# Optimization experiments

Measured on AMD Instinct MI355X. Metric: run time of the kernel, lower is better.

## Reference

```python
import jax, jax.numpy as jnp
import numpy as np

NO_LAYERS = 2048
MODES = 4096
APL = 8          # action_per_layer
BATCH = 1        # forced to 1 by the final .view on a batch-1 tensor


def setup_inputs() -> dict:
    key = jax.random.key(0)
    ks = jax.random.split(key, 12)

    def cplx(k, shape):
        k1, k2 = jax.random.split(k)
        return (jax.random.uniform(k1, shape) + 1j * jax.random.uniform(k2, shape)).astype(jnp.complex64)

    return {
        "model_p": jax.random.normal(ks[0], (NO_LAYERS, MODES), dtype=jnp.float32),
        # complex spectral weights, torch.rand init on cfloat -> uniform real+imag
        "w_fft_0": cplx(ks[1], (1, MODES)),
        "w_fft_1": cplx(ks[2], (1, MODES)),
        "w_fft_2": cplx(ks[3], (1, MODES)),
        # lin1: no_layers -> modes
        "lin1_w": jax.random.normal(ks[4], (MODES, NO_LAYERS), dtype=jnp.float32) / np.sqrt(NO_LAYERS),
        "lin1_b": jnp.zeros((MODES,), dtype=jnp.float32),
        # lin2: modes -> no_layers * action_per_layer  (the big matvec, 268 MB)
        "lin2_w": jax.random.normal(ks[5], (NO_LAYERS * APL, MODES), dtype=jnp.float32) / np.sqrt(MODES),
        "lin2_b": jnp.zeros((NO_LAYERS * APL,), dtype=jnp.float32),
    }


def _space_time_fft_feature(data, w_fft):
    # data: (b, f, p) real or complex; w_fft: (1, modes) complex
    fft_data = jnp.fft.fft(data, norm='forward')                 # (b, f, p)
    # einsum contracts both p and n, leaving singleton m -> (b, f, 1)
    y = jnp.einsum('bfp,mn->bfm', fft_data, w_fft)
    iffw = jnp.fft.ifft(y, norm='forward')                       # (b, f, 1)
    return jnp.tanh(iffw).real                                   # complex tanh, take real


def reference(model_p, w_fft_0, w_fft_1, w_fft_2, lin1_w, lin1_b, lin2_w, lin2_b):
    x = _space_time_fft_feature(model_p[None], w_fft_0)          # (1, no_layers, 1)
    x = _space_time_fft_feature(x, w_fft_1)                      # (1, no_layers, 1)
    x = _space_time_fft_feature(x, w_fft_2)                      # (1, no_layers, 1)
    x = x.reshape(1, -1)                                         # (1, no_layers)
    x = jnp.tanh(x @ lin1_w.T + lin1_b)                          # (1, modes)
    x = (x @ lin2_w.T + lin2_b).reshape(BATCH, NO_LAYERS, APL)   # (1, no_layers, apl)
    return x
```

## Files before the change

kernel.cpp:

```cpp
#include <hip/hip_runtime.h>
#include <math.h>

#define NO_LAYERS 2048
#define MODES 4096
#define APL 8
#define OUT_N (NO_LAYERS * APL)

typedef float nf4 __attribute__((ext_vector_type(4)));

__device__ __forceinline__ float retanh_cplx(float t, float Sr, float Si) {
    float x = t * Sr;
    float y = t * Si;
    float a = 2.0f * fabsf(x);
    float e1 = expf(-a);
    float e2 = e1 * e1;
    float num = 1.0f - e2;
    float den = 1.0f + e2 + 2.0f * e1 * cosf(2.0f * y);
    return copysignf(num / den, x);
}

__global__ void __launch_bounds__(256) k_lin1f(const float* __restrict__ model_p,
                                               const float* __restrict__ w0,
                                               const float* __restrict__ w1,
                                               const float* __restrict__ w2,
                                               const float* __restrict__ w,
                                               const float* __restrict__ b,
                                               float* __restrict__ h) {
    __shared__ float red[3][2][4];
    __shared__ float S[3][2];
    __shared__ float ts[NO_LAYERS];
    const int tid = threadIdx.x;
    const int wave = tid >> 6, lane = tid & 63;

    const int row = blockIdx.x * 4 + wave;
    const nf4* wp = (const nf4*)(w + (size_t)row * NO_LAYERS);
    nf4 wv[(NO_LAYERS / 4) / 64];
    #pragma unroll
    for (int i = 0; i < (NO_LAYERS / 4) / 64; i++)
        wv[i] = __builtin_nontemporal_load(&wp[i * 64 + lane]);

    const float* wptr[3] = {w0, w1, w2};
    float sr[3] = {0.f, 0.f, 0.f}, si[3] = {0.f, 0.f, 0.f};
    #pragma unroll
    for (int q = 0; q < 3; q++) {
        const float2* p = (const float2*)wptr[q];
        #pragma unroll
        for (int i = 0; i < MODES / 256; i++) {
            float2 v = p[i * 256 + tid];
            sr[q] += v.x; si[q] += v.y;
        }
    }
    #pragma unroll
    for (int off = 32; off > 0; off >>= 1) {
        #pragma unroll
        for (int q = 0; q < 3; q++) {
            sr[q] += __shfl_down(sr[q], off);
            si[q] += __shfl_down(si[q], off);
        }
    }
    if (lane == 0) {
        #pragma unroll
        for (int q = 0; q < 3; q++) { red[q][0][wave] = sr[q]; red[q][1][wave] = si[q]; }
    }
    __syncthreads();
    if (tid < 6) {
        int q = tid >> 1, c = tid & 1;
        S[q][c] = red[q][c][0] + red[q][c][1] + red[q][c][2] + red[q][c][3];
    }
    __syncthreads();
    const float S0r = S[0][0], S0i = S[0][1];
    const float S1r = S[1][0], S1i = S[1][1];
    const float S2r = S[2][0], S2i = S[2][1];

    #pragma unroll
    for (int k = 0; k < NO_LAYERS / 256; k++) {
        const int f = k * 256 + tid;
        float t = model_p[(size_t)f * MODES];
        t = retanh_cplx(t, S0r, S0i);
        t = retanh_cplx(t, S1r, S1i);
        t = retanh_cplx(t, S2r, S2i);
        ts[f] = t;
    }
    __syncthreads();

    const float4* tp = (const float4*)ts;
    float acc = 0.f;
    #pragma unroll
    for (int i = 0; i < (NO_LAYERS / 4) / 64; i++) {
        float4 tv = tp[i * 64 + lane];
        acc += wv[i].x * tv.x + wv[i].y * tv.y + wv[i].z * tv.z + wv[i].w * tv.w;
    }
    #pragma unroll
    for (int off = 32; off > 0; off >>= 1) acc += __shfl_down(acc, off);
    if (lane == 0) h[row] = tanhf(acc + b[row]);
}

__global__ void __launch_bounds__(256) k_lin2(const float* __restrict__ h,
                                              const float* __restrict__ w,
                                              const float* __restrict__ b,
                                              float* __restrict__ out) {
    __shared__ float hs[MODES];
    const int tid = threadIdx.x;
    const int wave = tid >> 6, lane = tid & 63;
    const int row0 = blockIdx.x * 8 + wave * 2;
    const nf4* wp0 = (const nf4*)(w + (size_t)row0 * MODES);
    const nf4* wp1 = (const nf4*)(w + (size_t)(row0 + 1) * MODES);

    nf4 pw0[4], pw1[4];
    #pragma unroll
    for (int i = 0; i < 4; i++) {
        pw0[i] = __builtin_nontemporal_load(&wp0[i * 64 + lane]);
        pw1[i] = __builtin_nontemporal_load(&wp1[i * 64 + lane]);
    }

    {
        const float4* hp = (const float4*)h;
        float4* sp = (float4*)hs;
        #pragma unroll
        for (int i = 0; i < (MODES / 4) / 256; i++) sp[i * 256 + tid] = hp[i * 256 + tid];
    }
    __syncthreads();

    const float4* hp = (const float4*)hs;
    float acc0 = 0.f, acc1 = 0.f;
    #pragma unroll
    for (int i = 0; i < 4; i++) {
        float4 hv = hp[i * 64 + lane];
        acc0 += pw0[i].x * hv.x + pw0[i].y * hv.y + pw0[i].z * hv.z + pw0[i].w * hv.w;
        acc1 += pw1[i].x * hv.x + pw1[i].y * hv.y + pw1[i].z * hv.z + pw1[i].w * hv.w;
    }
    #pragma unroll
    for (int i = 4; i < (MODES / 4) / 64; i++) {
        const int idx = i * 64 + lane;
        float4 hv = hp[idx];
        nf4 w0v = __builtin_nontemporal_load(&wp0[idx]);
        nf4 w1v = __builtin_nontemporal_load(&wp1[idx]);
        acc0 += w0v.x * hv.x + w0v.y * hv.y + w0v.z * hv.z + w0v.w * hv.w;
        acc1 += w1v.x * hv.x + w1v.y * hv.y + w1v.z * hv.z + w1v.w * hv.w;
    }
    #pragma unroll
    for (int off = 32; off > 0; off >>= 1) {
        acc0 += __shfl_down(acc0, off);
        acc1 += __shfl_down(acc1, off);
    }
    if (lane == 0) {
        out[row0]     = acc0 + b[row0];
        out[row0 + 1] = acc1 + b[row0 + 1];
    }
}

extern "C" void kernel_launch(void* const* d_in, const int* in_sizes, int n_in,
                              void* d_out, int out_size, void* d_ws, size_t ws_size,
                              hipStream_t stream) {
    const float* model_p = (const float*)d_in[0];
    const float* w0      = (const float*)d_in[1];
    const float* w1      = (const float*)d_in[2];
    const float* w2      = (const float*)d_in[3];
    const float* lin1_w  = (const float*)d_in[4];
    const float* lin1_b  = (const float*)d_in[5];
    const float* lin2_w  = (const float*)d_in[6];
    const float* lin2_b  = (const float*)d_in[7];
    float* out = (float*)d_out;

    float* h = (float*)d_ws;

    k_lin1f<<<1024, 256, 0, stream>>>(model_p, w0, w1, w2, lin1_w, lin1_b, h);
    k_lin2<<<2048, 256, 0, stream>>>(h, lin2_w, lin2_b, out);
}
```

Measured before the change: 387.4 us.

## Fuse lin1 and lin2 into one kernel with a global atomic grid barrier

Merges the lin1 and lin2 kernels into one persistent kernel of 1024 blocks. A global atomic counter acts as a grid barrier, so the hidden vector is ready before lin2 starts. Each wave now handles 4 lin2 rows, and their first weight chunks are prefetched before the barrier so the weight stream overlaps the wait. This removes the second launch and the gap between kernels, but the grid barrier assumes all 1024 blocks (4 per CU via launch bounds) are resident at once, and it adds a memset launch to reset the counter.

```diff
diff --git a/kernel.cpp b/kernel.cpp
--- a/kernel.cpp
+++ b/kernel.cpp
@@ -5,6 +5,7 @@
 #define MODES 4096
 #define APL 8
 #define OUT_N (NO_LAYERS * APL)
+#define NBLK 1024
 
 typedef float nf4 __attribute__((ext_vector_type(4)));
 
@@ -19,27 +20,31 @@
     return copysignf(num / den, x);
 }
 
-__global__ void __launch_bounds__(256) k_lin1f(const float* __restrict__ model_p,
-                                               const float* __restrict__ w0,
-                                               const float* __restrict__ w1,
-                                               const float* __restrict__ w2,
-                                               const float* __restrict__ w,
-                                               const float* __restrict__ b,
-                                               float* __restrict__ h) {
+__global__ void __launch_bounds__(256, 4)
+k_fused(const float* __restrict__ model_p,
+        const float* __restrict__ wf0,
+        const float* __restrict__ wf1,
+        const float* __restrict__ wf2,
+        const float* __restrict__ l1w,
+        const float* __restrict__ l1b,
+        const float* __restrict__ l2w,
+        const float* __restrict__ l2b,
+        float* __restrict__ h,
+        unsigned int* __restrict__ flag,
+        float* __restrict__ out) {
+    __shared__ float buf[MODES];
     __shared__ float red[3][2][4];
     __shared__ float S[3][2];
-    __shared__ float ts[NO_LAYERS];
     const int tid = threadIdx.x;
     const int wave = tid >> 6, lane = tid & 63;
 
-    const int row = blockIdx.x * 4 + wave;
-    const nf4* wp = (const nf4*)(w + (size_t)row * NO_LAYERS);
-    nf4 wv[(NO_LAYERS / 4) / 64];
+    const int r1 = blockIdx.x * 4 + wave;
+    const nf4* wp = (const nf4*)(l1w + (size_t)r1 * NO_LAYERS);
+    nf4 wv[8];
     #pragma unroll
-    for (int i = 0; i < (NO_LAYERS / 4) / 64; i++)
-        wv[i] = __builtin_nontemporal_load(&wp[i * 64 + lane]);
+    for (int i = 0; i < 8; i++) wv[i] = __builtin_nontemporal_load(&wp[i * 64 + lane]);
 
-    const float* wptr[3] = {w0, w1, w2};
+    const float* wptr[3] = {wf0, wf1, wf2};
     float sr[3] = {0.f, 0.f, 0.f}, si[3] = {0.f, 0.f, 0.f};
     #pragma unroll
     for (int q = 0; q < 3; q++) {
@@ -79,73 +84,87 @@
         t = retanh_cplx(t, S0r, S0i);
         t = retanh_cplx(t, S1r, S1i);
         t = retanh_cplx(t, S2r, S2i);
-        ts[f] = t;
+        buf[f] = t;
     }
     __syncthreads();
 
-    const float4* tp = (const float4*)ts;
-    float acc = 0.f;
+    {
+        const float4* tp = (const float4*)buf;
+        float acc = 0.f;
+        #pragma unroll
+        for (int i = 0; i < 8; i++) {
+            float4 tv = tp[i * 64 + lane];
+            acc += wv[i].x * tv.x + wv[i].y * tv.y + wv[i].z * tv.z + wv[i].w * tv.w;
+        }
+        #pragma unroll
+        for (int off = 32; off > 0; off >>= 1) acc += __shfl_down(acc, off);
+        if (lane == 0) h[r1] = tanhf(acc + l1b[r1]);
+    }
+
+    const int r2 = blockIdx.x * 16 + wave * 4;
+    const nf4* qv = (const nf4*)(l2w + (size_t)r2 * MODES);
+    nf4 pw[2][4];
     #pragma unroll
-    for (int i = 0; i < (NO_LAYERS / 4) / 64; i++) {
-        float4 tv = tp[i * 64 + lane];
-        acc += wv[i].x * tv.x + wv[i].y * tv.y + wv[i].z * tv.z + wv[i].w * tv.w;
+    for (int j = 0; j < 2; j++) {
+        const int idx = j * 64 + lane;
+        #pragma unroll
+        for (int r = 0; r < 4; r++)
+            pw[j][r] = __builtin_nontemporal_load(&qv[r * (MODES / 4) + idx]);
     }
-    #pragma unroll
-    for (int off = 32; off > 0; off >>= 1) acc += __shfl_down(acc, off);
-    if (lane == 0) h[row] = tanhf(acc + b[row]);
-}
 
-__global__ void __launch_bounds__(256) k_lin2(const float* __restrict__ h,
-                                              const float* __restrict__ w,
-                                              const float* __restrict__ b,
-                                              float* __restrict__ out) {
-    __shared__ float hs[MODES];
-    const int tid = threadIdx.x;
-    const int wave = tid >> 6, lane = tid & 63;
-    const int row0 = blockIdx.x * 8 + wave * 2;
-    const nf4* wp0 = (const nf4*)(w + (size_t)row0 * MODES);
-    const nf4* wp1 = (const nf4*)(w + (size_t)(row0 + 1) * MODES);
-
-    nf4 pw0[4], pw1[4];
-    #pragma unroll
-    for (int i = 0; i < 4; i++) {
-        pw0[i] = __builtin_nontemporal_load(&wp0[i * 64 + lane]);
-        pw1[i] = __builtin_nontemporal_load(&wp1[i * 64 + lane]);
+    __threadfence();
+    __syncthreads();
+    if (tid == 0) {
+        __hip_atomic_fetch_add(flag, 1u, __ATOMIC_RELEASE, __HIP_MEMORY_SCOPE_AGENT);
+        while (__hip_atomic_load(flag, __ATOMIC_ACQUIRE, __HIP_MEMORY_SCOPE_AGENT) < NBLK)
+            __builtin_amdgcn_s_sleep(2);
     }
+    __syncthreads();
+    __threadfence();
 
     {
         const float4* hp = (const float4*)h;
-        float4* sp = (float4*)hs;
+        float4* sp = (float4*)buf;
         #pragma unroll
         for (int i = 0; i < (MODES / 4) / 256; i++) sp[i * 256 + tid] = hp[i * 256 + tid];
     }
     __syncthreads();
 
-    const float4* hp = (const float4*)hs;
-    float acc0 = 0.f, acc1 = 0.f;
+    const float4* hb = (const float4*)buf;
+    float a0 = 0.f, a1 = 0.f, a2 = 0.f, a3 = 0.f;
     #pragma unroll
-    for (int i = 0; i < 4; i++) {
-        float4 hv = hp[i * 64 + lane];
-        acc0 += pw0[i].x * hv.x + pw0[i].y * hv.y + pw0[i].z * hv.z + pw0[i].w * hv.w;
-        acc1 += pw1[i].x * hv.x + pw1[i].y * hv.y + pw1[i].z * hv.z + pw1[i].w * hv.w;
+    for (int j = 0; j < 2; j++) {
+        float4 hv = hb[j * 64 + lane];
+        a0 += pw[j][0].x * hv.x + pw[j][0].y * hv.y + pw[j][0].z * hv.z + pw[j][0].w * hv.w;
+        a1 += pw[j][1].x * hv.x + pw[j][1].y * hv.y + pw[j][1].z * hv.z + pw[j][1].w * hv.w;
+        a2 += pw[j][2].x * hv.x + pw[j][2].y * hv.y + pw[j][2].z * hv.z + pw[j][2].w * hv.w;
+        a3 += pw[j][3].x * hv.x + pw[j][3].y * hv.y + pw[j][3].z * hv.z + pw[j][3].w * hv.w;
     }
-    #pragma unroll
-    for (int i = 4; i < (MODES / 4) / 64; i++) {
+    #pragma unroll 2
+    for (int i = 2; i < 16; i++) {
         const int idx = i * 64 + lane;
-        float4 hv = hp[idx];
-        nf4 w0v = __builtin_nontemporal_load(&wp0[idx]);
-        nf4 w1v = __builtin_nontemporal_load(&wp1[idx]);
-        acc0 += w0v.x * hv.x + w0v.y * hv.y + w0v.z * hv.z + w0v.w * hv.w;
-        acc1 += w1v.x * hv.x + w1v.y * hv.y + w1v.z * hv.z + w1v.w * hv.w;
+        float4 hv = hb[idx];
+        nf4 v0 = __builtin_nontemporal_load(&qv[0 * (MODES / 4) + idx]);
+        nf4 v1 = __builtin_nontemporal_load(&qv[1 * (MODES / 4) + idx]);
+        nf4 v2 = __builtin_nontemporal_load(&qv[2 * (MODES / 4) + idx]);
+        nf4 v3 = __builtin_nontemporal_load(&qv[3 * (MODES / 4) + idx]);
+        a0 += v0.x * hv.x + v0.y * hv.y + v0.z * hv.z + v0.w * hv.w;
+        a1 += v1.x * hv.x + v1.y * hv.y + v1.z * hv.z + v1.w * hv.w;
+        a2 += v2.x * hv.x + v2.y * hv.y + v2.z * hv.z + v2.w * hv.w;
+        a3 += v3.x * hv.x + v3.y * hv.y + v3.z * hv.z + v3.w * hv.w;
     }
     #pragma unroll
     for (int off = 32; off > 0; off >>= 1) {
-        acc0 += __shfl_down(acc0, off);
-        acc1 += __shfl_down(acc1, off);
+        a0 += __shfl_down(a0, off);
+        a1 += __shfl_down(a1, off);
+        a2 += __shfl_down(a2, off);
+        a3 += __shfl_down(a3, off);
     }
     if (lane == 0) {
-        out[row0]     = acc0 + b[row0];
-        out[row0 + 1] = acc1 + b[row0 + 1];
+        out[r2]     = a0 + l2b[r2];
+        out[r2 + 1] = a1 + l2b[r2 + 1];
+        out[r2 + 2] = a2 + l2b[r2 + 2];
+        out[r2 + 3] = a3 + l2b[r2 + 3];
     }
 }
 
@@ -153,9 +172,9 @@
                               void* d_out, int out_size, void* d_ws, size_t ws_size,
                               hipStream_t stream) {
     const float* model_p = (const float*)d_in[0];
-    const float* w0      = (const float*)d_in[1];
-    const float* w1      = (const float*)d_in[2];
-    const float* w2      = (const float*)d_in[3];
+    const float* wf0     = (const float*)d_in[1];
+    const float* wf1     = (const float*)d_in[2];
+    const float* wf2     = (const float*)d_in[3];
     const float* lin1_w  = (const float*)d_in[4];
     const float* lin1_b  = (const float*)d_in[5];
     const float* lin2_w  = (const float*)d_in[6];
@@ -163,7 +182,10 @@
     float* out = (float*)d_out;
 
     float* h = (float*)d_ws;
+    unsigned int* flag = (unsigned int*)((char*)d_ws + MODES * sizeof(float));
 
-    k_lin1f<<<1024, 256, 0, stream>>>(model_p, w0, w1, w2, lin1_w, lin1_b, h);
-    k_lin2<<<2048, 256, 0, stream>>>(h, lin2_w, lin2_b, out);
+    hipMemsetAsync(flag, 0, sizeof(unsigned int), stream);
+    k_fused<<<NBLK, 256, 0, stream>>>(model_p, wf0, wf1, wf2,
+                                      lin1_w, lin1_b, lin2_w, lin2_b,
+                                      h, flag, out);
 }
```

New measurement: 766.4 us. 97.8% more time.
